# Kernel tuning notes

Hardware: AMD Instinct MI355X
Metric: run time of the kernel (lower is better)

The kernel has to match this reference:

```python
import jax, jax.numpy as jnp
import numpy as np

B, C, H, N = 4, 128, 4, 2048
D = C // H  # head_dim = 32
BN_EPS = 1e-5


def _conv1(w, b, x):
    # 1x1 Conv1d: [O,C] x [B,C,N] -> [B,O,N]
    return jnp.einsum('oc,bcn->bon', w, x) + b[None, :, None]


def setup_inputs() -> dict:
    key = jax.random.key(0)
    ks = jax.random.split(key, 20)
    p = lambda k, shape: jax.random.normal(k, shape, dtype=jnp.float32) * 0.05
    return {
        'x1': jax.random.normal(ks[0], (B, C, N), dtype=jnp.float32),
        'x2': jax.random.normal(ks[1], (B, C, N), dtype=jnp.float32),
        'kv_mask': jnp.ones((B, N), dtype=bool),
        'wq': p(ks[2], (C, C)), 'bq': p(ks[3], (C,)),
        'wk': p(ks[4], (C, C)), 'bk': p(ks[5], (C,)),
        'wv': p(ks[6], (C, C)), 'bv': p(ks[7], (C,)),
        'wm': p(ks[8], (C, C)), 'bm': p(ks[9], (C,)),
        'wc1': p(ks[10], (2 * C, 2 * C)), 'bc1': p(ks[11], (2 * C,)),
        'bn_gamma': jnp.ones((2 * C,), dtype=jnp.float32),
        'bn_beta': jnp.zeros((2 * C,), dtype=jnp.float32),
        'bn_mean': p(ks[12], (2 * C,)),
        'bn_var': jax.random.uniform(ks[13], (2 * C,), dtype=jnp.float32, minval=0.5, maxval=1.5),
        'wc2': p(ks[14], (C, 2 * C)), 'bc2': p(ks[15], (C,)),
    }


def reference(x1, x2, kv_mask, wq, bq, wk, bk, wv, bv, wm, bm,
              wc1, bc1, bn_gamma, bn_beta, bn_mean, bn_var, wc2, bc2):
    b, _, n = x1.shape
    q = _conv1(wq, bq, x1).reshape(b, H, D, n)   # bhdn
    k = _conv1(wk, bk, x2).reshape(b, H, D, -1)  # bhdm
    v = _conv1(wv, bv, x2).reshape(b, H, D, -1)  # bhdm
    qk = jnp.einsum('bhdn,bhdm->bhnm', q, k)
    # masked_fill on raw QK before scaling, matching torch code
    qk = jnp.where(kv_mask[:, None, None, :], qk, jnp.float32(-1e6))
    score = jax.nn.softmax(qk * (1.0 / D ** 0.5), axis=-1)
    add_value = jnp.einsum('bhnm,bhdm->bhdn', score, v).reshape(b, C, n)
    add_value = _conv1(wm, bm, add_value)
    cat = jnp.concatenate([x1, add_value], axis=1)  # [B, 2C, N]
    h = _conv1(wc1, bc1, cat)
    # BatchNorm1d in inference mode (running stats)
    h = (h - bn_mean[None, :, None]) * jax.lax.rsqrt(bn_var[None, :, None] + BN_EPS)
    h = h * bn_gamma[None, :, None] + bn_beta[None, :, None]
    h = jax.nn.relu(h)
    h = _conv1(wc2, bc2, h)
    return x1 + h
```

## Files before the change

kernel.cpp:

```cpp
#include <hip/hip_runtime.h>

typedef __attribute__((ext_vector_type(4))) float v4f;
typedef __attribute__((ext_vector_type(8))) _Float16 half8;
typedef __attribute__((ext_vector_type(4))) _Float16 half4;
typedef __attribute__((ext_vector_type(2))) _Float16 half2t;

constexpr float C2 = 0.17677669529663687f * 1.44269504088896341f;

__device__ __forceinline__ half4 pk4(float a, float b, float c, float d) {
  half2t lo = __builtin_bit_cast(half2t, __builtin_amdgcn_cvt_pkrtz(a, b));
  half2t hi = __builtin_bit_cast(half2t, __builtin_amdgcn_cvt_pkrtz(c, d));
  return __builtin_shufflevector(lo, hi, 0, 1, 2, 3);
}
__device__ __forceinline__ half8 pk8f4(const float4 a, const float4 b) {
  const half4 lo = pk4(a.x, a.y, a.z, a.w);
  const half4 hi = pk4(b.x, b.y, b.z, b.w);
  return __builtin_shufflevector(lo, hi, 0, 1, 2, 3, 4, 5, 6, 7);
}

__global__ __launch_bounds__(512) void qkv(
    const float* __restrict__ x1, const float* __restrict__ x2,
    const float* __restrict__ wq, const float* __restrict__ bq,
    const float* __restrict__ wk, const float* __restrict__ bk,
    const float* __restrict__ wv, const float* __restrict__ bv,
    const float* __restrict__ wm, const float* __restrict__ wc1,
    const float* __restrict__ wc2, const unsigned char* __restrict__ mask,
    _Float16* __restrict__ Qpk, _Float16* __restrict__ Kpk,
    _Float16* __restrict__ Vpk, _Float16* __restrict__ wts,
    float* __restrict__ maskf) {
  const int b = blockIdx.y;
  const int bx = blockIdx.x;
  const int tid = threadIdx.x, w = tid >> 6, lane = tid & 63;
  const int l = lane & 15, q = lane >> 4;
  const int n0 = bx * 16;
  const int n = n0 + l;

  __shared__ _Float16 x1s[16 * 136];
  __shared__ _Float16 x2s[16 * 136];

  if (b == 0 && bx < 72) {
    const int e = (bx * 512 + tid) * 4;
    const float* src;
    int base;
    if (e < 16384) { src = wm; base = 0; }
    else if (e < 81920) { src = wc1; base = 16384; }
    else { src = wc2; base = 81920; }
    const float4 t = *(const float4*)(src + (e - base));
    *(half4*)(wts + e) = pk4(t.x, t.y, t.z, t.w);
  } else if (b == 1 && bx < 4) {
    const int e = (bx * 512 + tid) * 4;
    const unsigned mv = *(const unsigned*)(mask + e);
    float4 o;
    o.x = (mv & 0x000000ffu) ? 0.f : -1.0e6f * C2;
    o.y = (mv & 0x0000ff00u) ? 0.f : -1.0e6f * C2;
    o.z = (mv & 0x00ff0000u) ? 0.f : -1.0e6f * C2;
    o.w = (mv & 0xff000000u) ? 0.f : -1.0e6f * C2;
    *(float4*)(maskf + e) = o;
  }

  {
    const int ch = tid >> 2, seg = tid & 3;
    const float4 a = *(const float4*)(x1 + (size_t)(b * 128 + ch) * 2048 + n0 + seg * 4);
    const float4 c = *(const float4*)(x2 + (size_t)(b * 128 + ch) * 2048 + n0 + seg * 4);
    x1s[(seg * 4 + 0) * 136 + ch] = (_Float16)a.x;
    x1s[(seg * 4 + 1) * 136 + ch] = (_Float16)a.y;
    x1s[(seg * 4 + 2) * 136 + ch] = (_Float16)a.z;
    x1s[(seg * 4 + 3) * 136 + ch] = (_Float16)a.w;
    x2s[(seg * 4 + 0) * 136 + ch] = (_Float16)c.x;
    x2s[(seg * 4 + 1) * 136 + ch] = (_Float16)c.y;
    x2s[(seg * 4 + 2) * 136 + ch] = (_Float16)c.z;
    x2s[(seg * 4 + 3) * 136 + ch] = (_Float16)c.w;
  }
  __syncthreads();

  half8 x1f[4], x2f[4];
#pragma unroll
  for (int kt = 0; kt < 4; ++kt) {
    x1f[kt] = *(const half8*)&x1s[l * 136 + kt * 32 + q * 8];
    x2f[kt] = *(const half8*)&x2s[l * 136 + kt * 32 + q * 8];
  }

#pragma unroll
  for (int i = 0; i < 3; ++i) {
    const int t = w * 3 + i;
    if (t < 8) {
      const int mt = t;
      v4f acc = *(const v4f*)(bq + mt * 16 + q * 4);
#pragma unroll
      for (int kt = 0; kt < 4; ++kt) {
        const float4 wa = *(const float4*)(wq + (mt * 16 + l) * 128 + kt * 32 + q * 8);
        const float4 wb = *(const float4*)(wq + (mt * 16 + l) * 128 + kt * 32 + q * 8 + 4);
        acc = __builtin_amdgcn_mfma_f32_16x16x32_f16(pk8f4(wa, wb), x1f[kt], acc, 0, 0, 0);
      }
      *(half4*)(Qpk + ((size_t)(b * 8 + mt) * 2048 + n) * 16 + q * 4) =
          pk4(acc[0] * C2, acc[1] * C2, acc[2] * C2, acc[3] * C2);
    } else if (t < 16) {
      const int mt = t - 8;
      v4f acc = *(const v4f*)(bk + mt * 16 + q * 4);
#pragma unroll
      for (int kt = 0; kt < 4; ++kt) {
        const float4 wa = *(const float4*)(wk + (mt * 16 + l) * 128 + kt * 32 + q * 8);
        const float4 wb = *(const float4*)(wk + (mt * 16 + l) * 128 + kt * 32 + q * 8 + 4);
        acc = __builtin_amdgcn_mfma_f32_16x16x32_f16(pk8f4(wa, wb), x2f[kt], acc, 0, 0, 0);
      }
      *(half4*)(Kpk + ((size_t)(b * 8 + mt) * 2048 + n) * 16 + q * 4) =
          pk4(acc[0], acc[1], acc[2], acc[3]);
    } else {
      const int ot = t - 16;
      const float bvv = bv[ot * 16 + l];
      v4f acc = {bvv, bvv, bvv, bvv};
#pragma unroll
      for (int kt = 0; kt < 4; ++kt) {
        const float4 wa = *(const float4*)(wv + (ot * 16 + l) * 128 + kt * 32 + q * 8);
        const float4 wb = *(const float4*)(wv + (ot * 16 + l) * 128 + kt * 32 + q * 8 + 4);
        acc = __builtin_amdgcn_mfma_f32_16x16x32_f16(x2f[kt], pk8f4(wa, wb), acc, 0, 0, 0);
      }
      *(half4*)(Vpk + (((size_t)(b * 4 + (ot >> 1)) * 128 + bx) * 32 +
                       (ot & 1) * 16 + l) * 16 + q * 4) =
          pk4(acc[0], acc[1], acc[2], acc[3]);
    }
  }
}

__global__ __launch_bounds__(256) void attn(
    const _Float16* __restrict__ Qpk, const _Float16* __restrict__ Kpk,
    const _Float16* __restrict__ Vpk, const float* __restrict__ maskf,
    _Float16* __restrict__ Opk, float* __restrict__ lsump) {
  const int bh = blockIdx.y, b = bh >> 2, h = bh & 3;
  const int part = blockIdx.z;
  const int tid = threadIdx.x, w = tid >> 6, lane = tid & 63;
  const int l = lane & 15, q = lane >> 4;
  const int nb = blockIdx.x * 128 + w * 32;

  __shared__ _Float16 ldsK[2][3088];
  __shared__ _Float16 ldsV[2][3072];
  __shared__ __align__(16) float biass[512];

  const size_t qrow = (size_t)(b * 8 + h * 2 + (q >> 1)) * 2048;
  const half8 qf0 = *(const half8*)(Qpk + (qrow + nb + l) * 16 + (q & 1) * 8);
  const half8 qf1 = *(const half8*)(Qpk + (qrow + nb + 16 + l) * 16 + (q & 1) * 8);
  const _Float16* __restrict__ Kg = Kpk + (size_t)(b * 8 + h * 2) * 2048 * 16;
  const _Float16* __restrict__ Vg = Vpk + (size_t)((b * 4 + h) * 128) * 512;

  const int kct = tid >> 7, kk = (tid >> 1) & 63, khf = tid & 1;
  const int vt = tid >> 6, vd = (tid >> 1) & 31;

  v4f oacc[2][2] = {{{0.f, 0.f, 0.f, 0.f}, {0.f, 0.f, 0.f, 0.f}},
                    {{0.f, 0.f, 0.f, 0.f}, {0.f, 0.f, 0.f, 0.f}}};
  v4f lsacc[2] = {{0.f, 0.f, 0.f, 0.f}, {0.f, 0.f, 0.f, 0.f}};
  const half4 ones = {(_Float16)1.f, (_Float16)1.f, (_Float16)1.f, (_Float16)1.f};
  const int mbeg = part * 512;

  if (tid < 128)
    *(float4*)&biass[tid * 4] = *(const float4*)(maskf + b * 2048 + mbeg + tid * 4);
  half8 kr = *(const half8*)(Kg + ((size_t)kct * 2048 + mbeg + kk) * 16 + khf * 8);
  half8 vr = *(const half8*)(Vg + (size_t)((mbeg >> 4) + vt) * 512 + vd * 16 + khf * 8);
  *(half8*)&ldsK[0][kct * 1544 + kk * 24 + khf * 8] = kr;
  *(half8*)&ldsV[0][vt * 768 + vd * 24 + khf * 8] = vr;
  __syncthreads();

  for (int i = 0; i < 8; ++i) {
    const int m0 = mbeg + i * 64;
    const int cur = i & 1;
    if (i < 7) {
      kr = *(const half8*)(Kg + ((size_t)kct * 2048 + m0 + 64 + kk) * 16 + khf * 8);
      vr = *(const half8*)(Vg + (size_t)(((m0 + 64) >> 4) + vt) * 512 + vd * 16 + khf * 8);
    }
    half4 pB[2][4];
#pragma unroll
    for (int mt = 0; mt < 4; ++mt) {
      const half8 kf =
          *(const half8*)&ldsK[cur][(q >> 1) * 1544 + (mt * 16 + l) * 24 + (q & 1) * 8];
      const v4f biasv = *(const v4f*)&biass[i * 64 + mt * 16 + q * 4];
      __builtin_amdgcn_s_setprio(1);
      const v4f s0 = __builtin_amdgcn_mfma_f32_16x16x32_f16(kf, qf0, biasv, 0, 0, 0);
      const v4f s1 = __builtin_amdgcn_mfma_f32_16x16x32_f16(kf, qf1, biasv, 0, 0, 0);
      __builtin_amdgcn_s_setprio(0);
      const float a0 = exp2f(s0[0]), a1 = exp2f(s0[1]), a2 = exp2f(s0[2]),
                  a3 = exp2f(s0[3]);
      const float c0 = exp2f(s1[0]), c1 = exp2f(s1[1]), c2 = exp2f(s1[2]),
                  c3 = exp2f(s1[3]);
      pB[0][mt] = pk4(a0, a1, a2, a3);
      pB[1][mt] = pk4(c0, c1, c2, c3);
    }
    __builtin_amdgcn_s_setprio(1);
#pragma unroll
    for (int mt = 0; mt < 4; ++mt) {
      const half4 vf0 = *(const half4*)&ldsV[cur][mt * 768 + l * 24 + q * 4];
      const half4 vf1 = *(const half4*)&ldsV[cur][mt * 768 + (16 + l) * 24 + q * 4];
      oacc[0][0] = __builtin_amdgcn_mfma_f32_16x16x16f16(vf0, pB[0][mt], oacc[0][0], 0, 0, 0);
      oacc[0][1] = __builtin_amdgcn_mfma_f32_16x16x16f16(vf1, pB[0][mt], oacc[0][1], 0, 0, 0);
      oacc[1][0] = __builtin_amdgcn_mfma_f32_16x16x16f16(vf0, pB[1][mt], oacc[1][0], 0, 0, 0);
      oacc[1][1] = __builtin_amdgcn_mfma_f32_16x16x16f16(vf1, pB[1][mt], oacc[1][1], 0, 0, 0);
      lsacc[0] = __builtin_amdgcn_mfma_f32_16x16x16f16(ones, pB[0][mt], lsacc[0], 0, 0, 0);
      lsacc[1] = __builtin_amdgcn_mfma_f32_16x16x16f16(ones, pB[1][mt], lsacc[1], 0, 0, 0);
    }
    __builtin_amdgcn_s_setprio(0);
    if (i < 7) {
      *(half8*)&ldsK[cur ^ 1][kct * 1544 + kk * 24 + khf * 8] = kr;
      *(half8*)&ldsV[cur ^ 1][vt * 768 + vd * 24 + khf * 8] = vr;
      __syncthreads();
    }
  }
  if (q == 0) {
    lsump[part * 32768 + bh * 2048 + nb + l] = lsacc[0][0];
    lsump[part * 32768 + bh * 2048 + nb + 16 + l] = lsacc[1][0];
  }
#pragma unroll
  for (int qt = 0; qt < 2; ++qt)
#pragma unroll
    for (int df = 0; df < 2; ++df)
      *(half4*)(Opk + (size_t)part * 1048576 +
                ((size_t)(b * 8 + h * 2 + df) * 2048 + nb + qt * 16 + l) * 16 +
                q * 4) = pk4(oacc[qt][df][0], oacc[qt][df][1], oacc[qt][df][2],
                             oacc[qt][df][3]);
}

__global__ __launch_bounds__(512) void post(
    const float* __restrict__ x1, const _Float16* __restrict__ Opk,
    const float* __restrict__ lsump, const _Float16* __restrict__ wts,
    const float* __restrict__ bm, const float* __restrict__ bc1,
    const float* __restrict__ gamma, const float* __restrict__ beta,
    const float* __restrict__ mean, const float* __restrict__ var,
    const float* __restrict__ bc2, float* __restrict__ out) {
  const int b = blockIdx.y;
  const int n0 = blockIdx.x * 16;
  const int tid = threadIdx.x, w = tid >> 6, lane = tid & 63;
  const int l = lane & 15, q = lane >> 4;
  const int n = n0 + l;
  const _Float16* wm_h = wts;
  const _Float16* wc1_h = wts + 16384;
  const _Float16* wc2_h = wts + 81920;

  __shared__ __align__(16) float x1s[16 * 132];
  __shared__ __align__(16) _Float16 ofs[8 * 256];
  __shared__ __align__(16) _Float16 exA[8 * 256];
  __shared__ __align__(16) _Float16 exB[16 * 256];

  {
    const int ch = tid >> 2, seg = tid & 3;
    const float4 a = *(const float4*)(x1 + (size_t)(b * 128 + ch) * 2048 + n0 + seg * 4);
    x1s[(seg * 4 + 0) * 132 + ch] = a.x;
    x1s[(seg * 4 + 1) * 132 + ch] = a.y;
    x1s[(seg * 4 + 2) * 132 + ch] = a.z;
    x1s[(seg * 4 + 3) * 132 + ch] = a.w;
  }
  {
    const size_t idx = (size_t)(b * 4 + (w >> 1)) * 2048 + n;
    const float rl = 1.0f / (lsump[idx] + lsump[32768 + idx] +
                             lsump[65536 + idx] + lsump[98304 + idx]);
    const size_t oa = ((size_t)(b * 8 + w) * 2048 + n) * 16 + q * 4;
    const half4 a = *(const half4*)(Opk + oa);
    const half4 c = *(const half4*)(Opk + 1048576 + oa);
    const half4 d = *(const half4*)(Opk + 2097152 + oa);
    const half4 e = *(const half4*)(Opk + 3145728 + oa);
    const _Float16 rh = (_Float16)rl;
    const half4 rl4 = {rh, rh, rh, rh};
    *(half4*)&ofs[w * 256 + l * 16 + q * 4] = ((a + c) + (d + e)) * rl4;
  }
  __syncthreads();

  half4 of[8];
#pragma unroll
  for (int kt = 0; kt < 8; ++kt)
    of[kt] = *(const half4*)&ofs[kt * 256 + l * 16 + q * 4];
  half4 catf[16];
  float xr[4];
#pragma unroll
  for (int kt = 0; kt < 8; ++kt) {
    const float4 xv = *(const float4*)&x1s[l * 132 + kt * 16 + q * 4];
    if (kt == w) { xr[0] = xv.x; xr[1] = xv.y; xr[2] = xv.z; xr[3] = xv.w; }
    catf[kt] = pk4(xv.x, xv.y, xv.z, xv.w);
  }
  {
    v4f acc = *(const v4f*)(bm + w * 16 + q * 4);
#pragma unroll
    for (int kt = 0; kt < 8; ++kt) {
      const half4 wf = *(const half4*)(wm_h + (w * 16 + l) * 128 + kt * 16 + q * 4);
      acc = __builtin_amdgcn_mfma_f32_16x16x16f16(wf, of[kt], acc, 0, 0, 0);
    }
    *(half4*)&exA[w * 256 + l * 16 + q * 4] = pk4(acc[0], acc[1], acc[2], acc[3]);
  }
  __syncthreads();
#pragma unroll
  for (int f = 0; f < 8; ++f)
    catf[8 + f] = *(const half4*)&exA[f * 256 + l * 16 + q * 4];
#pragma unroll
  for (int i = 0; i < 2; ++i) {
    const int mt = w * 2 + i;
    v4f acc = *(const v4f*)(bc1 + mt * 16 + q * 4);
#pragma unroll
    for (int kt = 0; kt < 16; ++kt) {
      const half4 wf = *(const half4*)(wc1_h + (mt * 16 + l) * 256 + kt * 16 + q * 4);
      acc = __builtin_amdgcn_mfma_f32_16x16x16f16(wf, catf[kt], acc, 0, 0, 0);
    }
    const v4f g = *(const v4f*)(gamma + mt * 16 + q * 4);
    const v4f bt = *(const v4f*)(beta + mt * 16 + q * 4);
    const v4f mn = *(const v4f*)(mean + mt * 16 + q * 4);
    const v4f vr = *(const v4f*)(var + mt * 16 + q * 4);
    float hh[4];
#pragma unroll
    for (int r = 0; r < 4; ++r) {
      const float a1 = g[r] * rsqrtf(vr[r] + 1e-5f);
      const float b1 = bt[r] - mn[r] * a1;
      hh[r] = fmaxf(acc[r] * a1 + b1, 0.f);
    }
    *(half4*)&exB[mt * 256 + l * 16 + q * 4] = pk4(hh[0], hh[1], hh[2], hh[3]);
  }
  __syncthreads();
  {
    v4f acc = *(const v4f*)(bc2 + w * 16 + q * 4);
#pragma unroll
    for (int kt = 0; kt < 16; ++kt) {
      const half4 hfv = *(const half4*)&exB[kt * 256 + l * 16 + q * 4];
      const half4 wf = *(const half4*)(wc2_h + (w * 16 + l) * 256 + kt * 16 + q * 4);
      acc = __builtin_amdgcn_mfma_f32_16x16x16f16(wf, hfv, acc, 0, 0, 0);
    }
#pragma unroll
    for (int r = 0; r < 4; ++r)
      out[(size_t)(b * 128 + w * 16 + q * 4 + r) * 2048 + n] = acc[r] + xr[r];
  }
}

extern "C" void kernel_launch(void* const* d_in, const int* in_sizes, int n_in,
                              void* d_out, int out_size, void* d_ws,
                              size_t ws_size, hipStream_t stream) {
  const float* x1 = (const float*)d_in[0];
  const float* x2 = (const float*)d_in[1];
  const unsigned char* kv_mask = (const unsigned char*)d_in[2];
  const float* wq = (const float*)d_in[3];
  const float* bq = (const float*)d_in[4];
  const float* wk = (const float*)d_in[5];
  const float* bk = (const float*)d_in[6];
  const float* wv = (const float*)d_in[7];
  const float* bv = (const float*)d_in[8];
  const float* wm = (const float*)d_in[9];
  const float* bm = (const float*)d_in[10];
  const float* wc1 = (const float*)d_in[11];
  const float* bc1 = (const float*)d_in[12];
  const float* bn_gamma = (const float*)d_in[13];
  const float* bn_beta = (const float*)d_in[14];
  const float* bn_mean = (const float*)d_in[15];
  const float* bn_var = (const float*)d_in[16];
  const float* wc2 = (const float*)d_in[17];
  const float* bc2 = (const float*)d_in[18];
  float* out = (float*)d_out;

  char* p = (char*)d_ws;
  _Float16* Qpk = (_Float16*)p;
  _Float16* Kpk = (_Float16*)(p + (size_t)2 * 1024 * 1024);
  _Float16* Vpk = (_Float16*)(p + (size_t)4 * 1024 * 1024);
  _Float16* Opk = (_Float16*)(p + (size_t)6 * 1024 * 1024);
  _Float16* wts = (_Float16*)(p + (size_t)14 * 1024 * 1024);
  float* lsump = (float*)(p + (size_t)14 * 1024 * 1024 + 512 * 1024);
  float* maskf = lsump + 4 * 32768;

  qkv<<<dim3(128, 4), 512, 0, stream>>>(x1, x2, wq, bq, wk, bk, wv, bv, wm,
                                        wc1, wc2, kv_mask, Qpk, Kpk, Vpk, wts,
                                        maskf);
  attn<<<dim3(16, 16, 4), 256, 0, stream>>>(Qpk, Kpk, Vpk, maskf, Opk, lsump);
  post<<<dim3(128, 4), 512, 0, stream>>>(x1, Opk, lsump, wts, bm, bc1,
                                         bn_gamma, bn_beta, bn_mean, bn_var,
                                         bc2, out);
}
```

Baseline: 161.2 us.

## Process two 16-column groups per block in qkv and post kernels

The qkv and post kernels now handle 32 sequence columns per block instead of 16, halving the grid and reusing each converted weight fragment across two MFMA column groups. Weight and mask conversion work is redistributed across the smaller grid, and launch bounds request higher occupancy. Post now stages x1 in fp16 in shared memory instead of holding concat fragments in registers. This adds LDS usage and halves the block count, which may reduce parallelism on a large GPU.

New measurement: 143.1 us. -11.2%, faster.

```diff
diff --git a/kernel.cpp b/kernel.cpp
--- a/kernel.cpp
+++ b/kernel.cpp
@@ -18,7 +18,7 @@
   return __builtin_shufflevector(lo, hi, 0, 1, 2, 3, 4, 5, 6, 7);
 }
 
-__global__ __launch_bounds__(512) void qkv(
+__global__ __launch_bounds__(512, 4) void qkv(
     const float* __restrict__ x1, const float* __restrict__ x2,
     const float* __restrict__ wq, const float* __restrict__ bq,
     const float* __restrict__ wk, const float* __restrict__ bk,
@@ -32,13 +32,12 @@
   const int bx = blockIdx.x;
   const int tid = threadIdx.x, w = tid >> 6, lane = tid & 63;
   const int l = lane & 15, q = lane >> 4;
-  const int n0 = bx * 16;
-  const int n = n0 + l;
-
-  __shared__ _Float16 x1s[16 * 136];
-  __shared__ _Float16 x2s[16 * 136];
-
-  if (b == 0 && bx < 72) {
+  const int n0 = bx * 32;
+
+  __shared__ _Float16 x1s[2][16 * 136];
+  __shared__ _Float16 x2s[2][16 * 136];
+
+  if (b == 0) {
     const int e = (bx * 512 + tid) * 4;
     const float* src;
     int base;
@@ -47,7 +46,15 @@
     else { src = wc2; base = 81920; }
     const float4 t = *(const float4*)(src + (e - base));
     *(half4*)(wts + e) = pk4(t.x, t.y, t.z, t.w);
-  } else if (b == 1 && bx < 4) {
+  } else if (b == 1 && bx < 8) {
+    const int e = (((64 + bx) * 512) + tid) * 4;
+    const float* src;
+    int base;
+    if (e < 81920) { src = wc1; base = 16384; }
+    else { src = wc2; base = 81920; }
+    const float4 t = *(const float4*)(src + (e - base));
+    *(half4*)(wts + e) = pk4(t.x, t.y, t.z, t.w);
+  } else if (b == 2 && bx < 4) {
     const int e = (bx * 512 + tid) * 4;
     const unsigned mv = *(const unsigned*)(mask + e);
     float4 o;
@@ -60,64 +67,92 @@
 
   {
     const int ch = tid >> 2, seg = tid & 3;
-    const float4 a = *(const float4*)(x1 + (size_t)(b * 128 + ch) * 2048 + n0 + seg * 4);
-    const float4 c = *(const float4*)(x2 + (size_t)(b * 128 + ch) * 2048 + n0 + seg * 4);
-    x1s[(seg * 4 + 0) * 136 + ch] = (_Float16)a.x;
-    x1s[(seg * 4 + 1) * 136 + ch] = (_Float16)a.y;
-    x1s[(seg * 4 + 2) * 136 + ch] = (_Float16)a.z;
-    x1s[(seg * 4 + 3) * 136 + ch] = (_Float16)a.w;
-    x2s[(seg * 4 + 0) * 136 + ch] = (_Float16)c.x;
-    x2s[(seg * 4 + 1) * 136 + ch] = (_Float16)c.y;
-    x2s[(seg * 4 + 2) * 136 + ch] = (_Float16)c.z;
-    x2s[(seg * 4 + 3) * 136 + ch] = (_Float16)c.w;
-  }
-  __syncthreads();
-
-  half8 x1f[4], x2f[4];
-#pragma unroll
-  for (int kt = 0; kt < 4; ++kt) {
-    x1f[kt] = *(const half8*)&x1s[l * 136 + kt * 32 + q * 8];
-    x2f[kt] = *(const half8*)&x2s[l * 136 + kt * 32 + q * 8];
-  }
+#pragma unroll
+    for (int g = 0; g < 2; ++g) {
+      const float4 a =
+          *(const float4*)(x1 + (size_t)(b * 128 + ch) * 2048 + n0 + g * 16 + seg * 4);
+      const float4 c =
+          *(const float4*)(x2 + (size_t)(b * 128 + ch) * 2048 + n0 + g * 16 + seg * 4);
+      x1s[g][(seg * 4 + 0) * 136 + ch] = (_Float16)a.x;
+      x1s[g][(seg * 4 + 1) * 136 + ch] = (_Float16)a.y;
+      x1s[g][(seg * 4 + 2) * 136 + ch] = (_Float16)a.z;
+      x1s[g][(seg * 4 + 3) * 136 + ch] = (_Float16)a.w;
+      x2s[g][(seg * 4 + 0) * 136 + ch] = (_Float16)c.x;
+      x2s[g][(seg * 4 + 1) * 136 + ch] = (_Float16)c.y;
+      x2s[g][(seg * 4 + 2) * 136 + ch] = (_Float16)c.z;
+      x2s[g][(seg * 4 + 3) * 136 + ch] = (_Float16)c.w;
+    }
+  }
+  __syncthreads();
 
 #pragma unroll
   for (int i = 0; i < 3; ++i) {
     const int t = w * 3 + i;
     if (t < 8) {
       const int mt = t;
-      v4f acc = *(const v4f*)(bq + mt * 16 + q * 4);
+      half8 wf[4];
 #pragma unroll
       for (int kt = 0; kt < 4; ++kt) {
         const float4 wa = *(const float4*)(wq + (mt * 16 + l) * 128 + kt * 32 + q * 8);
         const float4 wb = *(const float4*)(wq + (mt * 16 + l) * 128 + kt * 32 + q * 8 + 4);
-        acc = __builtin_amdgcn_mfma_f32_16x16x32_f16(pk8f4(wa, wb), x1f[kt], acc, 0, 0, 0);
-      }
-      *(half4*)(Qpk + ((size_t)(b * 8 + mt) * 2048 + n) * 16 + q * 4) =
-          pk4(acc[0] * C2, acc[1] * C2, acc[2] * C2, acc[3] * C2);
+        wf[kt] = pk8f4(wa, wb);
+      }
+      const v4f bias = *(const v4f*)(bq + mt * 16 + q * 4);
+#pragma unroll
+      for (int g = 0; g < 2; ++g) {
+        v4f acc = bias;
+#pragma unroll
+        for (int kt = 0; kt < 4; ++kt) {
+          const half8 xf = *(const half8*)&x1s[g][l * 136 + kt * 32 + q * 8];
+          acc = __builtin_amdgcn_mfma_f32_16x16x32_f16(wf[kt], xf, acc, 0, 0, 0);
+        }
+        *(half4*)(Qpk + ((size_t)(b * 8 + mt) * 2048 + n0 + g * 16 + l) * 16 + q * 4) =
+            pk4(acc[0] * C2, acc[1] * C2, acc[2] * C2, acc[3] * C2);
+      }
     } else if (t < 16) {
       const int mt = t - 8;
-      v4f acc = *(const v4f*)(bk + mt * 16 + q * 4);
+      half8 wf[4];
 #pragma unroll
       for (int kt = 0; kt < 4; ++kt) {
         const float4 wa = *(const float4*)(wk + (mt * 16 + l) * 128 + kt * 32 + q * 8);
         const float4 wb = *(const float4*)(wk + (mt * 16 + l) * 128 + kt * 32 + q * 8 + 4);
-        acc = __builtin_amdgcn_mfma_f32_16x16x32_f16(pk8f4(wa, wb), x2f[kt], acc, 0, 0, 0);
-      }
-      *(half4*)(Kpk + ((size_t)(b * 8 + mt) * 2048 + n) * 16 + q * 4) =
-          pk4(acc[0], acc[1], acc[2], acc[3]);
+        wf[kt] = pk8f4(wa, wb);
+      }
+      const v4f bias = *(const v4f*)(bk + mt * 16 + q * 4);
+#pragma unroll
+      for (int g = 0; g < 2; ++g) {
+        v4f acc = bias;
+#pragma unroll
+        for (int kt = 0; kt < 4; ++kt) {
+          const half8 xf = *(const half8*)&x2s[g][l * 136 + kt * 32 + q * 8];
+          acc = __builtin_amdgcn_mfma_f32_16x16x32_f16(wf[kt], xf, acc, 0, 0, 0);
+        }
+        *(half4*)(Kpk + ((size_t)(b * 8 + mt) * 2048 + n0 + g * 16 + l) * 16 + q * 4) =
+            pk4(acc[0], acc[1], acc[2], acc[3]);
+      }
     } else {
       const int ot = t - 16;
-      const float bvv = bv[ot * 16 + l];
-      v4f acc = {bvv, bvv, bvv, bvv};
+      half8 wf[4];
 #pragma unroll
       for (int kt = 0; kt < 4; ++kt) {
         const float4 wa = *(const float4*)(wv + (ot * 16 + l) * 128 + kt * 32 + q * 8);
         const float4 wb = *(const float4*)(wv + (ot * 16 + l) * 128 + kt * 32 + q * 8 + 4);
-        acc = __builtin_amdgcn_mfma_f32_16x16x32_f16(x2f[kt], pk8f4(wa, wb), acc, 0, 0, 0);
-      }
-      *(half4*)(Vpk + (((size_t)(b * 4 + (ot >> 1)) * 128 + bx) * 32 +
-                       (ot & 1) * 16 + l) * 16 + q * 4) =
-          pk4(acc[0], acc[1], acc[2], acc[3]);
+        wf[kt] = pk8f4(wa, wb);
+      }
+      const float bvv = bv[ot * 16 + l];
+#pragma unroll
+      for (int g = 0; g < 2; ++g) {
+        v4f acc = {bvv, bvv, bvv, bvv};
+#pragma unroll
+        for (int kt = 0; kt < 4; ++kt) {
+          const half8 xf = *(const half8*)&x2s[g][l * 136 + kt * 32 + q * 8];
+          acc = __builtin_amdgcn_mfma_f32_16x16x32_f16(xf, wf[kt], acc, 0, 0, 0);
+        }
+        const int kx = bx * 2 + g;
+        *(half4*)(Vpk + (((size_t)(b * 4 + (ot >> 1)) * 128 + kx) * 32 +
+                         (ot & 1) * 16 + l) * 16 + q * 4) =
+            pk4(acc[0], acc[1], acc[2], acc[3]);
+      }
     }
   }
 }
@@ -216,7 +251,7 @@
                              oacc[qt][df][3]);
 }
 
-__global__ __launch_bounds__(512) void post(
+__global__ __launch_bounds__(512, 4) void post(
     const float* __restrict__ x1, const _Float16* __restrict__ Opk,
     const float* __restrict__ lsump, const _Float16* __restrict__ wts,
     const float* __restrict__ bm, const float* __restrict__ bc1,
@@ -224,101 +259,129 @@
     const float* __restrict__ mean, const float* __restrict__ var,
     const float* __restrict__ bc2, float* __restrict__ out) {
   const int b = blockIdx.y;
-  const int n0 = blockIdx.x * 16;
+  const int n0 = blockIdx.x * 32;
   const int tid = threadIdx.x, w = tid >> 6, lane = tid & 63;
   const int l = lane & 15, q = lane >> 4;
-  const int n = n0 + l;
   const _Float16* wm_h = wts;
   const _Float16* wc1_h = wts + 16384;
   const _Float16* wc2_h = wts + 81920;
 
-  __shared__ __align__(16) float x1s[16 * 132];
-  __shared__ __align__(16) _Float16 ofs[8 * 256];
-  __shared__ __align__(16) _Float16 exA[8 * 256];
-  __shared__ __align__(16) _Float16 exB[16 * 256];
+  __shared__ __align__(16) float x1s[2][16 * 132];
+  __shared__ __align__(16) _Float16 x1h[2][8 * 256];
+  __shared__ __align__(16) _Float16 ofs[2][8 * 256];
+  __shared__ __align__(16) _Float16 exA[2][8 * 256];
+  __shared__ __align__(16) _Float16 exB[2][16 * 256];
 
   {
     const int ch = tid >> 2, seg = tid & 3;
-    const float4 a = *(const float4*)(x1 + (size_t)(b * 128 + ch) * 2048 + n0 + seg * 4);
-    x1s[(seg * 4 + 0) * 132 + ch] = a.x;
-    x1s[(seg * 4 + 1) * 132 + ch] = a.y;
-    x1s[(seg * 4 + 2) * 132 + ch] = a.z;
-    x1s[(seg * 4 + 3) * 132 + ch] = a.w;
-  }
-  {
-    const size_t idx = (size_t)(b * 4 + (w >> 1)) * 2048 + n;
-    const float rl = 1.0f / (lsump[idx] + lsump[32768 + idx] +
-                             lsump[65536 + idx] + lsump[98304 + idx]);
-    const size_t oa = ((size_t)(b * 8 + w) * 2048 + n) * 16 + q * 4;
-    const half4 a = *(const half4*)(Opk + oa);
-    const half4 c = *(const half4*)(Opk + 1048576 + oa);
-    const half4 d = *(const half4*)(Opk + 2097152 + oa);
-    const half4 e = *(const half4*)(Opk + 3145728 + oa);
-    const _Float16 rh = (_Float16)rl;
-    const half4 rl4 = {rh, rh, rh, rh};
-    *(half4*)&ofs[w * 256 + l * 16 + q * 4] = ((a + c) + (d + e)) * rl4;
-  }
-  __syncthreads();
-
-  half4 of[8];
-#pragma unroll
-  for (int kt = 0; kt < 8; ++kt)
-    of[kt] = *(const half4*)&ofs[kt * 256 + l * 16 + q * 4];
-  half4 catf[16];
-  float xr[4];
-#pragma unroll
-  for (int kt = 0; kt < 8; ++kt) {
-    const float4 xv = *(const float4*)&x1s[l * 132 + kt * 16 + q * 4];
-    if (kt == w) { xr[0] = xv.x; xr[1] = xv.y; xr[2] = xv.z; xr[3] = xv.w; }
-    catf[kt] = pk4(xv.x, xv.y, xv.z, xv.w);
-  }
-  {
-    v4f acc = *(const v4f*)(bm + w * 16 + q * 4);
+#pragma unroll
+    for (int g = 0; g < 2; ++g) {
+      const float4 a =
+          *(const float4*)(x1 + (size_t)(b * 128 + ch) * 2048 + n0 + g * 16 + seg * 4);
+      x1s[g][(seg * 4 + 0) * 132 + ch] = a.x;
+      x1s[g][(seg * 4 + 1) * 132 + ch] = a.y;
+      x1s[g][(seg * 4 + 2) * 132 + ch] = a.z;
+      x1s[g][(seg * 4 + 3) * 132 + ch] = a.w;
+    }
+  }
+  {
+#pragma unroll
+    for (int g = 0; g < 2; ++g) {
+      const int n = n0 + g * 16 + l;
+      const size_t idx = (size_t)(b * 4 + (w >> 1)) * 2048 + n;
+      const float rl = 1.0f / (lsump[idx] + lsump[32768 + idx] +
+                               lsump[65536 + idx] + lsump[98304 + idx]);
+      const size_t oa = ((size_t)(b * 8 + w) * 2048 + n) * 16 + q * 4;
+      const half4 a = *(const half4*)(Opk + oa);
+      const half4 c = *(const half4*)(Opk + 1048576 + oa);
+      const half4 d = *(const half4*)(Opk + 2097152 + oa);
+      const half4 e = *(const half4*)(Opk + 3145728 + oa);
+      const _Float16 rh = (_Float16)rl;
+      const half4 rl4 = {rh, rh, rh, rh};
+      *(half4*)&ofs[g][w * 256 + l * 16 + q * 4] = ((a + c) + (d + e)) * rl4;
+    }
+  }
+  __syncthreads();
+  {
+#pragma unroll
+    for (int g = 0; g < 2; ++g) {
+      const float4 xv = *(const float4*)&x1s[g][l * 132 + w * 16 + q * 4];
+      *(half4*)&x1h[g][w * 256 + l * 16 + q * 4] = pk4(xv.x, xv.y, xv.z, xv.w);
+    }
+  }
+  __syncthreads();
+
+  {
+    const v4f bias = *(const v4f*)(bm + w * 16 + q * 4);
+    v4f acc[2] = {bias, bias};
 #pragma unroll
     for (int kt = 0; kt < 8; ++kt) {
       const half4 wf = *(const half4*)(wm_h + (w * 16 + l) * 128 + kt * 16 + q * 4);
-      acc = __builtin_amdgcn_mfma_f32_16x16x16f16(wf, of[kt], acc, 0, 0, 0);
-    }
-    *(half4*)&exA[w * 256 + l * 16 + q * 4] = pk4(acc[0], acc[1], acc[2], acc[3]);
-  }
-  __syncthreads();
-#pragma unroll
-  for (int f = 0; f < 8; ++f)
-    catf[8 + f] = *(const half4*)&exA[f * 256 + l * 16 + q * 4];
+#pragma unroll
+      for (int g = 0; g < 2; ++g) {
+        const half4 of = *(const half4*)&ofs[g][kt * 256 + l * 16 + q * 4];
+        acc[g] = __builtin_amdgcn_mfma_f32_16x16x16f16(wf, of, acc[g], 0, 0, 0);
+      }
+    }
+#pragma unroll
+    for (int g = 0; g < 2; ++g)
+      *(half4*)&exA[g][w * 256 + l * 16 + q * 4] =
+          pk4(acc[g][0], acc[g][1], acc[g][2], acc[g][3]);
+  }
+  __syncthreads();
 #pragma unroll
   for (int i = 0; i < 2; ++i) {
     const int mt = w * 2 + i;
-    v4f acc = *(const v4f*)(bc1 + mt * 16 + q * 4);
+    const v4f bias = *(const v4f*)(bc1 + mt * 16 + q * 4);
+    v4f acc[2] = {bias, bias};
 #pragma unroll
     for (int kt = 0; kt < 16; ++kt) {
       const half4 wf = *(const half4*)(wc1_h + (mt * 16 + l) * 256 + kt * 16 + q * 4);
-      acc = __builtin_amdgcn_mfma_f32_16x16x16f16(wf, catf[kt], acc, 0, 0, 0);
-    }
-    const v4f g = *(const v4f*)(gamma + mt * 16 + q * 4);
+#pragma unroll
+      for (int g = 0; g < 2; ++g) {
+        const half4 frag =
+            (kt < 8) ? *(const half4*)&x1h[g][kt * 256 + l * 16 + q * 4]
+                     : *(const half4*)&exA[g][(kt - 8) * 256 + l * 16 + q * 4];
+        acc[g] = __builtin_amdgcn_mfma_f32_16x16x16f16(wf, frag, acc[g], 0, 0, 0);
+      }
+    }
+    const v4f gm = *(const v4f*)(gamma + mt * 16 + q * 4);
     const v4f bt = *(const v4f*)(beta + mt * 16 + q * 4);
     const v4f mn = *(const v4f*)(mean + mt * 16 + q * 4);
     const v4f vr = *(const v4f*)(var + mt * 16 + q * 4);
-    float hh[4];
-#pragma unroll
-    for (int r = 0; r < 4; ++r) {
-      const float a1 = g[r] * rsqrtf(vr[r] + 1e-5f);
-      const float b1 = bt[r] - mn[r] * a1;
-      hh[r] = fmaxf(acc[r] * a1 + b1, 0.f);
-    }
-    *(half4*)&exB[mt * 256 + l * 16 + q * 4] = pk4(hh[0], hh[1], hh[2], hh[3]);
-  }
-  __syncthreads();
-  {
-    v4f acc = *(const v4f*)(bc2 + w * 16 + q * 4);
+#pragma unroll
+    for (int g = 0; g < 2; ++g) {
+      float hh[4];
+#pragma unroll
+      for (int r = 0; r < 4; ++r) {
+        const float a1 = gm[r] * rsqrtf(vr[r] + 1e-5f);
+        const float b1 = bt[r] - mn[r] * a1;
+        hh[r] = fmaxf(acc[g][r] * a1 + b1, 0.f);
+      }
+      *(half4*)&exB[g][mt * 256 + l * 16 + q * 4] = pk4(hh[0], hh[1], hh[2], hh[3]);
+    }
+  }
+  __syncthreads();
+  {
+    const v4f bias = *(const v4f*)(bc2 + w * 16 + q * 4);
+    v4f acc[2] = {bias, bias};
 #pragma unroll
     for (int kt = 0; kt < 16; ++kt) {
-      const half4 hfv = *(const half4*)&exB[kt * 256 + l * 16 + q * 4];
       const half4 wf = *(const half4*)(wc2_h + (w * 16 + l) * 256 + kt * 16 + q * 4);
-      acc = __builtin_amdgcn_mfma_f32_16x16x16f16(wf, hfv, acc, 0, 0, 0);
-    }
-#pragma unroll
-    for (int r = 0; r < 4; ++r)
-      out[(size_t)(b * 128 + w * 16 + q * 4 + r) * 2048 + n] = acc[r] + xr[r];
+#pragma unroll
+      for (int g = 0; g < 2; ++g) {
+        const half4 hfv = *(const half4*)&exB[g][kt * 256 + l * 16 + q * 4];
+        acc[g] = __builtin_amdgcn_mfma_f32_16x16x16f16(wf, hfv, acc[g], 0, 0, 0);
+      }
+    }
+#pragma unroll
+    for (int g = 0; g < 2; ++g) {
+      const int n = n0 + g * 16 + l;
+#pragma unroll
+      for (int r = 0; r < 4; ++r)
+        out[(size_t)(b * 128 + w * 16 + q * 4 + r) * 2048 + n] =
+            acc[g][r] + x1s[g][l * 132 + w * 16 + q * 4 + r];
+    }
   }
 }
 
@@ -355,11 +418,11 @@
   float* lsump = (float*)(p + (size_t)14 * 1024 * 1024 + 512 * 1024);
   float* maskf = lsump + 4 * 32768;
 
-  qkv<<<dim3(128, 4), 512, 0, stream>>>(x1, x2, wq, bq, wk, bk, wv, bv, wm,
-                                        wc1, wc2, kv_mask, Qpk, Kpk, Vpk, wts,
-                                        maskf);
+  qkv<<<dim3(64, 4), 512, 0, stream>>>(x1, x2, wq, bq, wk, bk, wv, bv, wm,
+                                       wc1, wc2, kv_mask, Qpk, Kpk, Vpk, wts,
+                                       maskf);
   attn<<<dim3(16, 16, 4), 256, 0, stream>>>(Qpk, Kpk, Vpk, maskf, Opk, lsump);
-  post<<<dim3(128, 4), 512, 0, stream>>>(x1, Opk, lsump, wts, bm, bc1,
-                                         bn_gamma, bn_beta, bn_mean, bn_var,
-                                         bc2, out);
-}
+  post<<<dim3(64, 4), 512, 0, stream>>>(x1, Opk, lsump, wts, bm, bc1,
+                                        bn_gamma, bn_beta, bn_mean, bn_var,
+                                        bc2, out);
+}
```
